# Performance work log

Measured on AMD Instinct MI355X. Metric: run time of the kernel, lower is better.

The kernel has to match this reference:

```python
import jax, jax.numpy as jnp
import numpy as np

N_NODES = 100000
N_EDGES = 640000
D_FEAT = 128
HIDDEN = 128
FINAL = 64
N_GRAPHS = 128


def setup_inputs() -> dict:
    key = jax.random.key(0)
    ks = jax.random.split(key, 8)
    x = jax.random.normal(ks[0], (N_NODES, D_FEAT), dtype=jnp.float32)
    edge_index = jax.random.randint(ks[1], (2, N_EDGES), 0, N_NODES, dtype=jnp.int64)
    batch = jnp.sort(jax.random.randint(ks[2], (N_NODES,), 0, N_GRAPHS, dtype=jnp.int64))
    # SAGEConv params: lin_l (aggregated neighbors, with bias), lin_r (self, no bias)
    W_l = jax.random.normal(ks[3], (HIDDEN, D_FEAT), dtype=jnp.float32) / np.sqrt(D_FEAT)
    b_l = jnp.zeros((HIDDEN,), dtype=jnp.float32)
    W_r = jax.random.normal(ks[4], (HIDDEN, D_FEAT), dtype=jnp.float32) / np.sqrt(D_FEAT)
    # Final linear head on column_stack([max_pool, mean_pool])
    W_lin = jax.random.normal(ks[5], (FINAL, 2 * HIDDEN), dtype=jnp.float32) / np.sqrt(2 * HIDDEN)
    b_lin = jnp.zeros((FINAL,), dtype=jnp.float32)
    return {"x": x, "edge_index": edge_index, "batch": batch,
            "W_l": W_l, "b_l": b_l, "W_r": W_r, "W_lin": W_lin, "b_lin": b_lin}


def reference(x, edge_index, batch, W_l, b_l, W_r, W_lin, b_lin):
    N = x.shape[0]
    src, dst = edge_index[0], edge_index[1]
    # SAGEConv: mean-aggregate neighbor messages src -> dst
    agg = jax.ops.segment_sum(x[src], dst, num_segments=N)  # [N, D]
    deg = jax.ops.segment_sum(jnp.ones_like(src, dtype=x.dtype), dst, num_segments=N)
    agg = agg / jnp.maximum(deg, 1.0)[:, None]
    h = agg @ W_l.T + b_l + x @ W_r.T  # [N, HIDDEN]
    h = jax.nn.relu(h)
    # global max / mean pool over graphs in batch
    x_max = jax.ops.segment_max(h, batch, num_segments=N_GRAPHS)  # [G, HIDDEN]
    cnt = jax.ops.segment_sum(jnp.ones((N,), h.dtype), batch, num_segments=N_GRAPHS)
    x_mean = jax.ops.segment_sum(h, batch, num_segments=N_GRAPHS) / jnp.maximum(cnt, 1.0)[:, None]
    z = jnp.concatenate([x_max, x_mean], axis=1)  # [G, 2*HIDDEN]
    # dropout is identity in eval mode (training=False)
    return z @ W_lin.T + b_lin
```

## Files before the change

kernel.cpp:

```cpp
#include <hip/hip_runtime.h>
#include <math.h>

#define NN 100000
#define NE 640000
#define DF 128
#define NG 128
#define NF 64
#define MAXDEG 32

typedef __attribute__((ext_vector_type(8))) short short8;
typedef __attribute__((ext_vector_type(4))) float floatx4;

__device__ __forceinline__ unsigned short bf16_rne(float v) {
    unsigned u = __float_as_uint(v);
    return (unsigned short)((u + 0x7FFF + ((u >> 16) & 1)) >> 16);
}

__global__ __launch_bounds__(256) void k_bucket(const int* __restrict__ ei,
                                                int* __restrict__ cnt,
                                                int* __restrict__ slot) {
    int e = blockIdx.x * 256 + threadIdx.x;
    if (e >= NE) return;
    int src = ei[e];
    int dst = ei[NE + e];
    int pos = atomicAdd(&cnt[dst], 1);
    if (pos < MAXDEG) slot[dst * MAXDEG + pos] = src;
}

__global__ __launch_bounds__(256) void k_aggregate(const float* __restrict__ x,
                                                   const int* __restrict__ slot,
                                                   const int* __restrict__ cnt,
                                                   float* __restrict__ agg) {
    int node = blockIdx.x * 4 + (threadIdx.x >> 6);
    int lane = threadIdx.x & 63;
    if (node >= NN) return;
    int g = lane >> 4, i = lane & 15;
    int myidx = (lane < MAXDEG) ? slot[node * MAXDEG + lane] : 0;
    int c = cnt[node];
    if (c > MAXDEG) c = MAXDEG;
    const float4* x4 = (const float4*)x;
    float4 a0 = make_float4(0.f, 0.f, 0.f, 0.f);
    float4 a1 = make_float4(0.f, 0.f, 0.f, 0.f);
    for (int e = g; e < c; e += 4) {
        int s = __shfl(myidx, e);
        size_t base = (size_t)s * 32 + i * 2;
        float4 v0 = x4[base];
        float4 v1 = x4[base + 1];
        a0.x += v0.x; a0.y += v0.y; a0.z += v0.z; a0.w += v0.w;
        a1.x += v1.x; a1.y += v1.y; a1.z += v1.z; a1.w += v1.w;
    }
    #pragma unroll
    for (int k = 16; k <= 32; k <<= 1) {
        a0.x += __shfl_xor(a0.x, k); a0.y += __shfl_xor(a0.y, k);
        a0.z += __shfl_xor(a0.z, k); a0.w += __shfl_xor(a0.w, k);
        a1.x += __shfl_xor(a1.x, k); a1.y += __shfl_xor(a1.y, k);
        a1.z += __shfl_xor(a1.z, k); a1.w += __shfl_xor(a1.w, k);
    }
    if (g == 0) {
        float4* agg4 = (float4*)agg;
        size_t base = (size_t)node * 32 + i * 2;
        agg4[base] = a0;
        agg4[base + 1] = a1;
    }
}

__global__ __launch_bounds__(256) void k_prepW(const float* __restrict__ Wl,
                                               const float* __restrict__ Wr,
                                               unsigned short* __restrict__ Bhi,
                                               unsigned short* __restrict__ Blo) {
    int idx = blockIdx.x * 256 + threadIdx.x;
    if (idx >= 256 * 128) return;
    int k = idx >> 7;
    int j = idx & 127;
    float v = (k < 128) ? Wl[j * 128 + k] : Wr[j * 128 + (k - 128)];
    int c = k >> 5, nb = j >> 4;
    int l = (j & 15) + (((k >> 3) & 3) << 4);
    int e = k & 7;
    int off = ((c * 8 + nb) * 64 + l) * 8 + e;
    unsigned short hb = bf16_rne(v);
    float hf = __uint_as_float((unsigned)hb << 16);
    Bhi[off] = hb;
    Blo[off] = bf16_rne(v - hf);
}

__global__ __launch_bounds__(256) void k_gemm_mfma(const float* __restrict__ agg,
                                                   const float* __restrict__ x,
                                                   const int* __restrict__ cnt,
                                                   const int* __restrict__ batch,
                                                   const unsigned short* __restrict__ Bhi,
                                                   const unsigned short* __restrict__ Blo,
                                                   const float* __restrict__ bl,
                                                   float* __restrict__ pmax,
                                                   float* __restrict__ psum) {
    __shared__ unsigned short Ahi_s[4 * 64 * 8];
    __shared__ unsigned short Alo_s[4 * 64 * 8];
    __shared__ float invd[64];
    __shared__ int sbatch[64];
    __shared__ float h_tile[64][132];
    int tid = threadIdx.x;
    int n0 = blockIdx.x * 64;
    if (tid < 64) {
        int node = n0 + tid;
        invd[tid]   = (node < NN) ? 1.f / fmaxf((float)cnt[node], 1.f) : 0.f;
        sbatch[tid] = (node < NN) ? batch[node] : -1;
    }
    int wave = tid >> 6, lane = tid & 63;
    int wm = wave >> 1, wn = wave & 1;

    floatx4 acc[2][4];
    #pragma unroll
    for (int m = 0; m < 2; ++m)
        #pragma unroll
        for (int n = 0; n < 4; ++n)
            acc[m][n] = (floatx4){0.f, 0.f, 0.f, 0.f};
    __syncthreads();

    for (int c = 0; c < 8; ++c) {
        const float* src = (c < 4) ? agg : x;
        int kbase = (c & 3) * 32;
        bool scale = (c < 4);
        #pragma unroll
        for (int i = 0; i < 2; ++i) {
            int idx = tid + i * 256;
            int row = idx >> 3, k4 = idx & 7;
            int node = n0 + row;
            float4 v = make_float4(0.f, 0.f, 0.f, 0.f);
            if (node < NN) v = *(const float4*)&src[(size_t)node * 128 + kbase + k4 * 4];
            float s = scale ? invd[row] : 1.f;
            v.x *= s; v.y *= s; v.z *= s; v.w *= s;
            int mb = row >> 4;
            int l  = (row & 15) + ((k4 >> 1) << 4);
            int base = ((mb << 6) + l) * 8 + ((k4 & 1) << 2);
            unsigned short h0 = bf16_rne(v.x), h1 = bf16_rne(v.y),
                           h2 = bf16_rne(v.z), h3 = bf16_rne(v.w);
            ushort4 hi4 = {h0, h1, h2, h3};
            ushort4 lo4 = {bf16_rne(v.x - __uint_as_float((unsigned)h0 << 16)),
                           bf16_rne(v.y - __uint_as_float((unsigned)h1 << 16)),
                           bf16_rne(v.z - __uint_as_float((unsigned)h2 << 16)),
                           bf16_rne(v.w - __uint_as_float((unsigned)h3 << 16))};
            *(ushort4*)&Ahi_s[base] = hi4;
            *(ushort4*)&Alo_s[base] = lo4;
        }
        __syncthreads();
        short8 ah[2], al[2];
        #pragma unroll
        for (int m = 0; m < 2; ++m) {
            int mb = wm * 2 + m;
            ah[m] = *(const short8*)&Ahi_s[((mb << 6) + lane) * 8];
            al[m] = *(const short8*)&Alo_s[((mb << 6) + lane) * 8];
        }
        #pragma unroll
        for (int n = 0; n < 4; ++n) {
            int nb = wn * 4 + n;
            int off = ((c * 8 + nb) * 64 + lane) * 8;
            short8 bh = *(const short8*)&Bhi[off];
            short8 bo = *(const short8*)&Blo[off];
            #pragma unroll
            for (int m = 0; m < 2; ++m) {
                acc[m][n] = __builtin_amdgcn_mfma_f32_16x16x32_bf16(ah[m], bh, acc[m][n], 0, 0, 0);
                acc[m][n] = __builtin_amdgcn_mfma_f32_16x16x32_bf16(ah[m], bo, acc[m][n], 0, 0, 0);
                acc[m][n] = __builtin_amdgcn_mfma_f32_16x16x32_bf16(al[m], bh, acc[m][n], 0, 0, 0);
            }
        }
        __syncthreads();
    }
    #pragma unroll
    for (int n = 0; n < 4; ++n) {
        int nb = wn * 4 + n;
        int col = nb * 16 + (lane & 15);
        float bv = bl[col];
        #pragma unroll
        for (int m = 0; m < 2; ++m) {
            int mb = wm * 2 + m;
            #pragma unroll
            for (int r = 0; r < 4; ++r) {
                int row = mb * 16 + ((lane >> 4) << 2) + r;
                h_tile[row][col] = fmaxf(acc[m][n][r] + bv, 0.f);
            }
        }
    }
    __syncthreads();
    {
        int col = tid & 127, half = tid >> 7;
        float mx = 0.f, sm = 0.f;
        int gcur = -2;
        for (int r = half * 32; r < half * 32 + 32; ++r) {
            int gb = sbatch[r];
            if (gb != gcur) {
                if (gcur >= 0) {
                    atomicMax((unsigned*)&pmax[gcur * 128 + col], __float_as_uint(mx));
                    atomicAdd(&psum[gcur * 128 + col], sm);
                }
                gcur = gb; mx = 0.f; sm = 0.f;
            }
            if (gb >= 0) {
                float v = h_tile[r][col];
                mx = fmaxf(mx, v);
                sm += v;
            }
        }
        if (gcur >= 0) {
            atomicMax((unsigned*)&pmax[gcur * 128 + col], __float_as_uint(mx));
            atomicAdd(&psum[gcur * 128 + col], sm);
        }
    }
}

__global__ __launch_bounds__(128) void k_pool2head(const float* __restrict__ pmax,
                                                   const float* __restrict__ psum,
                                                   const int* __restrict__ batch,
                                                   const float* __restrict__ Wlin,
                                                   const float* __restrict__ blin,
                                                   float* __restrict__ out) {
    int g = blockIdx.x;
    int t = threadIdx.x;
    int lo = 0, hi = NN;
    while (lo < hi) { int mid = (lo + hi) >> 1; if (batch[mid] < g) lo = mid + 1; else hi = mid; }
    int start = lo;
    hi = NN;
    while (lo < hi) { int mid = (lo + hi) >> 1; if (batch[mid] < g + 1) lo = mid + 1; else hi = mid; }
    int cntg = lo - start;
    __shared__ float z[256];
    z[t]       = pmax[g * 128 + t];
    z[128 + t] = psum[g * 128 + t] / fmaxf((float)cntg, 1.f);
    __syncthreads();
    if (t < 64) {
        float acc = blin[t];
        const float* w = &Wlin[t * 256];
        #pragma unroll 8
        for (int c = 0; c < 256; ++c) acc = fmaf(z[c], w[c], acc);
        out[g * 64 + t] = acc;
    }
}

extern "C" void kernel_launch(void* const* d_in, const int* in_sizes, int n_in,
                              void* d_out, int out_size, void* d_ws, size_t ws_size,
                              hipStream_t stream) {
    const float* x     = (const float*)d_in[0];
    const int*   ei    = (const int*)d_in[1];
    const int*   batch = (const int*)d_in[2];
    const float* Wl    = (const float*)d_in[3];
    const float* bl    = (const float*)d_in[4];
    const float* Wr    = (const float*)d_in[5];
    const float* Wlin  = (const float*)d_in[6];
    const float* blin  = (const float*)d_in[7];
    float* out = (float*)d_out;

    char* ws = (char*)d_ws;
    int*   cnt  = (int*)(ws);
    int*   slot = (int*)(ws + 409600);
    float* agg  = (float*)(ws + 13209600);
    float* pmax = (float*)(ws + 64409600);
    float* psum = (float*)(ws + 64475136);
    unsigned short* Bhi = (unsigned short*)(ws + 64540672);
    unsigned short* Blo = (unsigned short*)(ws + 64606208);

    hipMemsetAsync(cnt, 0, NN * sizeof(int), stream);
    hipMemsetAsync(pmax, 0, NG * 128 * sizeof(float), stream);
    hipMemsetAsync(psum, 0, NG * 128 * sizeof(float), stream);
    k_prepW<<<128, 256, 0, stream>>>(Wl, Wr, Bhi, Blo);
    k_bucket<<<NE / 256, 256, 0, stream>>>(ei, cnt, slot);
    k_aggregate<<<NN / 4, 256, 0, stream>>>(x, slot, cnt, agg);
    k_gemm_mfma<<<(NN + 63) / 64, 256, 0, stream>>>(agg, x, cnt, batch, Bhi, Blo, bl, pmax, psum);
    k_pool2head<<<NG, 128, 0, stream>>>(pmax, psum, batch, Wlin, blin, out);
}
```

Before: 239.9 us.

## Fuse neighbor aggregation into MFMA GEMM and pool kernel, dropping agg buffer

Merges the gather/mean aggregation kernel into the GEMM kernel. Each block aggregates 32 nodes directly into bf16 hi/lo split tiles in LDS, stages the self features the same way, then runs the full-K MFMA without per-chunk syncs. This removes the 51MB agg write and re-read and one launch. Pooling now uses in-register shuffle reductions per graph instead of an LDS h tile. In exchange, each block holds fewer rows, and threads walk neighbor lists up to the max count in each 16-lane group.

```diff
diff --git a/kernel.cpp b/kernel.cpp
--- a/kernel.cpp
+++ b/kernel.cpp
@@ -3,7 +3,6 @@
 
 #define NN 100000
 #define NE 640000
-#define DF 128
 #define NG 128
 #define NF 64
 #define MAXDEG 32
@@ -14,6 +13,13 @@
 __device__ __forceinline__ unsigned short bf16_rne(float v) {
     unsigned u = __float_as_uint(v);
     return (unsigned short)((u + 0x7FFF + ((u >> 16) & 1)) >> 16);
+}
+__device__ __forceinline__ void split2(float f0, float f1, unsigned& H, unsigned& L) {
+    unsigned short h0 = bf16_rne(f0), h1 = bf16_rne(f1);
+    float r0 = f0 - __uint_as_float((unsigned)h0 << 16);
+    float r1 = f1 - __uint_as_float((unsigned)h1 << 16);
+    H = (unsigned)h0 | ((unsigned)h1 << 16);
+    L = (unsigned)bf16_rne(r0) | ((unsigned)bf16_rne(r1) << 16);
 }
 
 __global__ __launch_bounds__(256) void k_bucket(const int* __restrict__ ei,
@@ -25,43 +31,6 @@
     int dst = ei[NE + e];
     int pos = atomicAdd(&cnt[dst], 1);
     if (pos < MAXDEG) slot[dst * MAXDEG + pos] = src;
-}
-
-__global__ __launch_bounds__(256) void k_aggregate(const float* __restrict__ x,
-                                                   const int* __restrict__ slot,
-                                                   const int* __restrict__ cnt,
-                                                   float* __restrict__ agg) {
-    int node = blockIdx.x * 4 + (threadIdx.x >> 6);
-    int lane = threadIdx.x & 63;
-    if (node >= NN) return;
-    int g = lane >> 4, i = lane & 15;
-    int myidx = (lane < MAXDEG) ? slot[node * MAXDEG + lane] : 0;
-    int c = cnt[node];
-    if (c > MAXDEG) c = MAXDEG;
-    const float4* x4 = (const float4*)x;
-    float4 a0 = make_float4(0.f, 0.f, 0.f, 0.f);
-    float4 a1 = make_float4(0.f, 0.f, 0.f, 0.f);
-    for (int e = g; e < c; e += 4) {
-        int s = __shfl(myidx, e);
-        size_t base = (size_t)s * 32 + i * 2;
-        float4 v0 = x4[base];
-        float4 v1 = x4[base + 1];
-        a0.x += v0.x; a0.y += v0.y; a0.z += v0.z; a0.w += v0.w;
-        a1.x += v1.x; a1.y += v1.y; a1.z += v1.z; a1.w += v1.w;
-    }
-    #pragma unroll
-    for (int k = 16; k <= 32; k <<= 1) {
-        a0.x += __shfl_xor(a0.x, k); a0.y += __shfl_xor(a0.y, k);
-        a0.z += __shfl_xor(a0.z, k); a0.w += __shfl_xor(a0.w, k);
-        a1.x += __shfl_xor(a1.x, k); a1.y += __shfl_xor(a1.y, k);
-        a1.z += __shfl_xor(a1.z, k); a1.w += __shfl_xor(a1.w, k);
-    }
-    if (g == 0) {
-        float4* agg4 = (float4*)agg;
-        size_t base = (size_t)node * 32 + i * 2;
-        agg4[base] = a0;
-        agg4[base + 1] = a1;
-    }
 }
 
 __global__ __launch_bounds__(256) void k_prepW(const float* __restrict__ Wl,
@@ -83,125 +52,118 @@
     Blo[off] = bf16_rne(v - hf);
 }
 
-__global__ __launch_bounds__(256) void k_gemm_mfma(const float* __restrict__ agg,
-                                                   const float* __restrict__ x,
-                                                   const int* __restrict__ cnt,
-                                                   const int* __restrict__ batch,
-                                                   const unsigned short* __restrict__ Bhi,
-                                                   const unsigned short* __restrict__ Blo,
-                                                   const float* __restrict__ bl,
-                                                   float* __restrict__ pmax,
-                                                   float* __restrict__ psum) {
-    __shared__ unsigned short Ahi_s[4 * 64 * 8];
-    __shared__ unsigned short Alo_s[4 * 64 * 8];
-    __shared__ float invd[64];
-    __shared__ int sbatch[64];
-    __shared__ float h_tile[64][132];
+__global__ __launch_bounds__(256) void k_fused(const float* __restrict__ x,
+                                               const int* __restrict__ slot,
+                                               const int* __restrict__ cnt,
+                                               const int* __restrict__ batch,
+                                               const unsigned short* __restrict__ Bhi,
+                                               const unsigned short* __restrict__ Blo,
+                                               const float* __restrict__ bl,
+                                               float* __restrict__ pmax,
+                                               float* __restrict__ psum) {
+    __shared__ unsigned short Ahi_s[2 * 8 * 64 * 8];
+    __shared__ unsigned short Alo_s[2 * 8 * 64 * 8];
+    __shared__ int sbatch[32];
     int tid = threadIdx.x;
-    int n0 = blockIdx.x * 64;
-    if (tid < 64) {
-        int node = n0 + tid;
-        invd[tid]   = (node < NN) ? 1.f / fmaxf((float)cnt[node], 1.f) : 0.f;
-        sbatch[tid] = (node < NN) ? batch[node] : -1;
-    }
     int wave = tid >> 6, lane = tid & 63;
+    int g = lane >> 4, i = lane & 15;
+    int n0 = blockIdx.x * 32;
+    if (tid < 32) sbatch[tid] = batch[n0 + tid];
+
+    const float4* x4 = (const float4*)x;
+    for (int p = 0; p < 2; ++p) {
+        int ln = wave * 8 + p * 4 + g;
+        int n = n0 + ln;
+        int ctrue = cnt[n];
+        float inv = 1.f / fmaxf((float)ctrue, 1.f);
+        int c = ctrue > MAXDEG ? MAXDEG : ctrue;
+        int idx0 = slot[n * MAXDEG + i];
+        int idx1 = slot[n * MAXDEG + 16 + i];
+        int cmax = c;
+        cmax = max(cmax, __shfl_xor(cmax, 16));
+        cmax = max(cmax, __shfl_xor(cmax, 32));
+        float4 a0 = make_float4(0.f, 0.f, 0.f, 0.f);
+        float4 a1 = make_float4(0.f, 0.f, 0.f, 0.f);
+        for (int e = 0; e < cmax; ++e) {
+            int s = (e < 16) ? __shfl(idx0, (lane & 48) + e)
+                             : __shfl(idx1, (lane & 48) + (e - 16));
+            if (e < c) {
+                float4 v0 = x4[(size_t)s * 32 + 2 * i];
+                float4 v1 = x4[(size_t)s * 32 + 2 * i + 1];
+                a0.x += v0.x; a0.y += v0.y; a0.z += v0.z; a0.w += v0.w;
+                a1.x += v1.x; a1.y += v1.y; a1.z += v1.z; a1.w += v1.w;
+            }
+        }
+        a0.x *= inv; a0.y *= inv; a0.z *= inv; a0.w *= inv;
+        a1.x *= inv; a1.y *= inv; a1.z *= inv; a1.w *= inv;
+        int base = (((ln >> 4) * 8 + (i >> 2)) * 64 + (ln & 15) + ((i & 3) << 4)) * 8;
+        uint4 H, L;
+        split2(a0.x, a0.y, H.x, L.x);
+        split2(a0.z, a0.w, H.y, L.y);
+        split2(a1.x, a1.y, H.z, L.z);
+        split2(a1.z, a1.w, H.w, L.w);
+        *(uint4*)&Ahi_s[base] = H;
+        *(uint4*)&Alo_s[base] = L;
+        float4 s0 = x4[(size_t)n * 32 + 2 * i];
+        float4 s1 = x4[(size_t)n * 32 + 2 * i + 1];
+        split2(s0.x, s0.y, H.x, L.x);
+        split2(s0.z, s0.w, H.y, L.y);
+        split2(s1.x, s1.y, H.z, L.z);
+        split2(s1.z, s1.w, H.w, L.w);
+        *(uint4*)&Ahi_s[base + 4 * 64 * 8] = H;
+        *(uint4*)&Alo_s[base + 4 * 64 * 8] = L;
+    }
+    __syncthreads();
+
     int wm = wave >> 1, wn = wave & 1;
-
-    floatx4 acc[2][4];
-    #pragma unroll
-    for (int m = 0; m < 2; ++m)
-        #pragma unroll
-        for (int n = 0; n < 4; ++n)
-            acc[m][n] = (floatx4){0.f, 0.f, 0.f, 0.f};
-    __syncthreads();
-
+    floatx4 acc[4];
+    #pragma unroll
+    for (int n = 0; n < 4; ++n) acc[n] = (floatx4){0.f, 0.f, 0.f, 0.f};
+    #pragma unroll
     for (int c = 0; c < 8; ++c) {
-        const float* src = (c < 4) ? agg : x;
-        int kbase = (c & 3) * 32;
-        bool scale = (c < 4);
-        #pragma unroll
-        for (int i = 0; i < 2; ++i) {
-            int idx = tid + i * 256;
-            int row = idx >> 3, k4 = idx & 7;
-            int node = n0 + row;
-            float4 v = make_float4(0.f, 0.f, 0.f, 0.f);
-            if (node < NN) v = *(const float4*)&src[(size_t)node * 128 + kbase + k4 * 4];
-            float s = scale ? invd[row] : 1.f;
-            v.x *= s; v.y *= s; v.z *= s; v.w *= s;
-            int mb = row >> 4;
-            int l  = (row & 15) + ((k4 >> 1) << 4);
-            int base = ((mb << 6) + l) * 8 + ((k4 & 1) << 2);
-            unsigned short h0 = bf16_rne(v.x), h1 = bf16_rne(v.y),
-                           h2 = bf16_rne(v.z), h3 = bf16_rne(v.w);
-            ushort4 hi4 = {h0, h1, h2, h3};
-            ushort4 lo4 = {bf16_rne(v.x - __uint_as_float((unsigned)h0 << 16)),
-                           bf16_rne(v.y - __uint_as_float((unsigned)h1 << 16)),
-                           bf16_rne(v.z - __uint_as_float((unsigned)h2 << 16)),
-                           bf16_rne(v.w - __uint_as_float((unsigned)h3 << 16))};
-            *(ushort4*)&Ahi_s[base] = hi4;
-            *(ushort4*)&Alo_s[base] = lo4;
-        }
-        __syncthreads();
-        short8 ah[2], al[2];
-        #pragma unroll
-        for (int m = 0; m < 2; ++m) {
-            int mb = wm * 2 + m;
-            ah[m] = *(const short8*)&Ahi_s[((mb << 6) + lane) * 8];
-            al[m] = *(const short8*)&Alo_s[((mb << 6) + lane) * 8];
-        }
+        short8 ah = *(const short8*)&Ahi_s[((wm * 8 + c) * 64 + lane) * 8];
+        short8 al = *(const short8*)&Alo_s[((wm * 8 + c) * 64 + lane) * 8];
         #pragma unroll
         for (int n = 0; n < 4; ++n) {
             int nb = wn * 4 + n;
             int off = ((c * 8 + nb) * 64 + lane) * 8;
             short8 bh = *(const short8*)&Bhi[off];
             short8 bo = *(const short8*)&Blo[off];
-            #pragma unroll
-            for (int m = 0; m < 2; ++m) {
-                acc[m][n] = __builtin_amdgcn_mfma_f32_16x16x32_bf16(ah[m], bh, acc[m][n], 0, 0, 0);
-                acc[m][n] = __builtin_amdgcn_mfma_f32_16x16x32_bf16(ah[m], bo, acc[m][n], 0, 0, 0);
-                acc[m][n] = __builtin_amdgcn_mfma_f32_16x16x32_bf16(al[m], bh, acc[m][n], 0, 0, 0);
-            }
+            acc[n] = __builtin_amdgcn_mfma_f32_16x16x32_bf16(ah, bh, acc[n], 0, 0, 0);
+            acc[n] = __builtin_amdgcn_mfma_f32_16x16x32_bf16(ah, bo, acc[n], 0, 0, 0);
+            acc[n] = __builtin_amdgcn_mfma_f32_16x16x32_bf16(al, bh, acc[n], 0, 0, 0);
         }
-        __syncthreads();
-    }
+    }
+
+    int colb = wn * 64 + i;
+    float v[4][4];
     #pragma unroll
     for (int n = 0; n < 4; ++n) {
-        int nb = wn * 4 + n;
-        int col = nb * 16 + (lane & 15);
-        float bv = bl[col];
+        float bv = bl[colb + n * 16];
         #pragma unroll
-        for (int m = 0; m < 2; ++m) {
-            int mb = wm * 2 + m;
+        for (int r = 0; r < 4; ++r) v[n][r] = fmaxf(acc[n][r] + bv, 0.f);
+    }
+    int myg[4];
+    #pragma unroll
+    for (int r = 0; r < 4; ++r) myg[r] = sbatch[wm * 16 + g * 4 + r];
+    int gfirst = sbatch[wm * 16];
+    int glast  = sbatch[wm * 16 + 15];
+    for (int gg = gfirst; gg <= glast; ++gg) {
+        #pragma unroll
+        for (int n = 0; n < 4; ++n) {
+            float mx = 0.f, sm = 0.f;
             #pragma unroll
             for (int r = 0; r < 4; ++r) {
-                int row = mb * 16 + ((lane >> 4) << 2) + r;
-                h_tile[row][col] = fmaxf(acc[m][n][r] + bv, 0.f);
+                if (myg[r] == gg) { mx = fmaxf(mx, v[n][r]); sm += v[n][r]; }
             }
-        }
-    }
-    __syncthreads();
-    {
-        int col = tid & 127, half = tid >> 7;
-        float mx = 0.f, sm = 0.f;
-        int gcur = -2;
-        for (int r = half * 32; r < half * 32 + 32; ++r) {
-            int gb = sbatch[r];
-            if (gb != gcur) {
-                if (gcur >= 0) {
-                    atomicMax((unsigned*)&pmax[gcur * 128 + col], __float_as_uint(mx));
-                    atomicAdd(&psum[gcur * 128 + col], sm);
-                }
-                gcur = gb; mx = 0.f; sm = 0.f;
+            mx = fmaxf(mx, __shfl_xor(mx, 16));
+            mx = fmaxf(mx, __shfl_xor(mx, 32));
+            sm += __shfl_xor(sm, 16);
+            sm += __shfl_xor(sm, 32);
+            if (lane < 16) {
+                atomicMax((unsigned*)&pmax[gg * 128 + colb + n * 16], __float_as_uint(mx));
+                atomicAdd(&psum[gg * 128 + colb + n * 16], sm);
             }
-            if (gb >= 0) {
-                float v = h_tile[r][col];
-                mx = fmaxf(mx, v);
-                sm += v;
-            }
-        }
-        if (gcur >= 0) {
-            atomicMax((unsigned*)&pmax[gcur * 128 + col], __float_as_uint(mx));
-            atomicAdd(&psum[gcur * 128 + col], sm);
         }
     }
 }
@@ -249,18 +211,16 @@
     char* ws = (char*)d_ws;
     int*   cnt  = (int*)(ws);
     int*   slot = (int*)(ws + 409600);
-    float* agg  = (float*)(ws + 13209600);
-    float* pmax = (float*)(ws + 64409600);
-    float* psum = (float*)(ws + 64475136);
-    unsigned short* Bhi = (unsigned short*)(ws + 64540672);
-    unsigned short* Blo = (unsigned short*)(ws + 64606208);
+    float* pmax = (float*)(ws + 13209600);
+    float* psum = (float*)(ws + 13275136);
+    unsigned short* Bhi = (unsigned short*)(ws + 13340672);
+    unsigned short* Blo = (unsigned short*)(ws + 13406208);
 
     hipMemsetAsync(cnt, 0, NN * sizeof(int), stream);
     hipMemsetAsync(pmax, 0, NG * 128 * sizeof(float), stream);
     hipMemsetAsync(psum, 0, NG * 128 * sizeof(float), stream);
     k_prepW<<<128, 256, 0, stream>>>(Wl, Wr, Bhi, Blo);
     k_bucket<<<NE / 256, 256, 0, stream>>>(ei, cnt, slot);
-    k_aggregate<<<NN / 4, 256, 0, stream>>>(x, slot, cnt, agg);
-    k_gemm_mfma<<<(NN + 63) / 64, 256, 0, stream>>>(agg, x, cnt, batch, Bhi, Blo, bl, pmax, psum);
+    k_fused<<<NN / 32, 256, 0, stream>>>(x, slot, cnt, batch, Bhi, Blo, bl, pmax, psum);
     k_pool2head<<<NG, 128, 0, stream>>>(pmax, psum, batch, Wlin, blin, out);
 }
```

After: 229.9 us. -4.2%, faster.
